# Kernel tuning notes

Measured on AMD Instinct MI355X. Metric: run time of the kernel, lower is better.

Reference implementation:

```python
import jax, jax.numpy as jnp
import numpy as np

B, N, D, H = 256, 64, 128, 64

def _w(key, shape, fan_in):
    return jax.random.normal(key, shape, jnp.float32) * (1.0 / np.sqrt(fan_in))

def setup_inputs() -> dict:
    key = jax.random.key(0)
    ks = jax.random.split(key, 6)
    return {
        "observations": jax.random.normal(ks[0], (B, N, D), jnp.float32),
        "enc_w": _w(ks[1], (D, H), D), "enc_b": jnp.zeros((H,), jnp.float32),
        "gate_w1": _w(ks[2], (2 * H, H), 2 * H), "gate_b1": jnp.zeros((H,), jnp.float32),
        "gate_w2": _w(ks[3], (H, 1), H), "gate_b2": jnp.zeros((1,), jnp.float32),
        "msg_w1": _w(ks[4], (H, H), H), "msg_b1": jnp.zeros((H,), jnp.float32),
        "msg_w2": _w(ks[5], (H, H), H), "msg_b2": jnp.zeros((H,), jnp.float32),
    }

def reference(observations, enc_w, enc_b, gate_w1, gate_b1, gate_w2, gate_b2,
              msg_w1, msg_b1, msg_w2, msg_b2):
    # encoder: (B, N, H)
    enc = jax.nn.relu(observations @ enc_w + enc_b)
    h = enc.shape[-1]
    # gate layer 1 on concat([e_i, e_j]) == e_i @ W_top + e_j @ W_bot; avoids
    # materializing the (B, N, N, 2H) concat tensor.
    w_i, w_j = gate_w1[:h], gate_w1[h:]
    gi = enc @ w_i                       # (B, N, H) contribution of receiver i
    gj = enc @ w_j + gate_b1             # (B, N, H) contribution of sender j
    hid = jax.nn.relu(gi[:, :, None, :] + gj[:, None, :, :])   # (B, N, N, H)
    gates = jax.nn.sigmoid(jnp.squeeze(hid @ gate_w2, -1) + gate_b2[0])  # (B, N, N)
    # message_gen(encoded): identical for every i in the original loop
    msg = jax.nn.relu(enc @ msg_w1 + msg_b1) @ msg_w2 + msg_b2  # (B, N, H)
    # enhanced[b, i] = sum_j gates[b, i, j] * msg[b, j]
    enhanced = jnp.einsum('bij,bjh->bih', gates, msg)           # (B, N, H)
    return enhanced
```

## Files before the change

### kernel.cpp

```cpp
#include <hip/hip_runtime.h>

typedef float  f32x4  __attribute__((ext_vector_type(4)));
typedef short  bf16x8 __attribute__((ext_vector_type(8)));

#define Bb 256

__device__ __forceinline__ uint cvtpk(float lo, float hi) {
    uint r;
    asm("v_cvt_pk_bf16_f32 %0, %1, %2" : "=v"(r) : "v"(lo), "v"(hi));
    return r;
}
__device__ __forceinline__ ushort f2b1(float v) { return (ushort)cvtpk(v, v); }

__device__ __forceinline__ void gl_lds16(const void* g, void* l) {
    __builtin_amdgcn_global_load_lds(
        (const __attribute__((address_space(1))) unsigned int*)g,
        (__attribute__((address_space(3))) unsigned int*)l, 16, 0, 0);
}

union U8 { uint u[4]; bf16x8 v; };

__global__ __launch_bounds__(256) void gcm_prep(
    const float* __restrict__ obs, const float* __restrict__ enc_w,
    const float* __restrict__ gate_w1, const float* __restrict__ msg_w1,
    const float* __restrict__ msg_w2,
    ushort* __restrict__ obs_bf, ushort* __restrict__ wimg)
{
    const int bid = blockIdx.x, t = threadIdx.x;
    if (bid < 1024) {
        const int G  = bid * 256 + t;
        const int e0 = G * 8;
        const int b  = e0 >> 13;
        const int r  = (e0 >> 7) & 63;
        const int d0 = e0 & 127;
        const int ds = d0 ^ ((r & 7) << 3);
        const float* src = obs + (((size_t)b * 64 + r) * 128 + ds);
        float4 f0 = *(const float4*)src;
        float4 f1 = *(const float4*)(src + 4);
        uint4 o;
        o.x = cvtpk(f0.x, f0.y); o.y = cvtpk(f0.z, f0.w);
        o.z = cvtpk(f1.x, f1.y); o.w = cvtpk(f1.z, f1.w);
        *(uint4*)(obs_bf + e0) = o;
    } else {
        const int G  = (bid - 1024) * 256 + t;
        const int e0 = G * 8;
        float v[8];
        if (e0 < 8192) {
            const int n  = e0 >> 7;
            const int k0 = (e0 & 127) ^ ((n & 7) << 3);
            #pragma unroll
            for (int j = 0; j < 8; ++j) v[j] = enc_w[(k0 + j) * 64 + n];
        } else {
            const int e  = e0 - 8192;
            const int n  = e >> 6;
            const int k0 = (e & 63) ^ ((n & 7) << 3);
            const float* base; int col;
            if (n < 64)       { base = gate_w1;           col = n;       }
            else if (n < 128) { base = gate_w1 + 64 * 64; col = n - 64;  }
            else if (n < 192) { base = msg_w1;            col = n - 128; }
            else              { base = msg_w2;            col = n - 192; }
            #pragma unroll
            for (int j = 0; j < 8; ++j) v[j] = base[(k0 + j) * 64 + col];
        }
        uint4 o;
        o.x = cvtpk(v[0], v[1]); o.y = cvtpk(v[2], v[3]);
        o.z = cvtpk(v[4], v[5]); o.w = cvtpk(v[6], v[7]);
        *(uint4*)(wimg + e0) = o;
    }
}

__global__ __launch_bounds__(1024, 1) void gcm_main(
    const ushort* __restrict__ obs_bf, const ushort* __restrict__ wimg,
    const float* __restrict__ enc_b, const float* __restrict__ gate_b1,
    const float* __restrict__ gate_w2, const float* __restrict__ gate_b2,
    const float* __restrict__ msg_b1, const float* __restrict__ msg_b2,
    float* __restrict__ out)
{
    const int bb   = blockIdx.x;
    const int t    = threadIdx.x;
    const int lane = t & 63;
    const int wv   = t >> 6;
    const int lr   = lane & 15;
    const int lg   = lane >> 4;
    const int rt   = wv & 3;
    const int ct   = wv >> 2;

    __shared__ __align__(16) char arena[131072];
    ushort* s_obs    = (ushort*)(arena);
    ushort* s_encwT  = (ushort*)(arena + 16384);
    ushort* s_wT     = (ushort*)(arena + 32768);
    ushort* s_enc    = (ushort*)(arena + 65536);
    ushort* s_msgh   = (ushort*)(arena + 73728);
    float*  s_gi     = (float*) (arena + 81920);
    float*  s_gj     = (float*) (arena + 98304);
    ushort* s_msgT   = (ushort*)(arena + 114688);
    ushort* s_gatesb = (ushort*)(arena + 122880);

    {
        const ushort* ob = obs_bf + (size_t)bb * 8192 + wv * 512 + lane * 8;
        gl_lds16(ob, arena + wv * 1024);
        const ushort* ew = wimg + wv * 512 + lane * 8;
        gl_lds16(ew, arena + 16384 + wv * 1024);
        const ushort* w0 = wimg + 8192 + wv * 512 + lane * 8;
        gl_lds16(w0, arena + 32768 + wv * 1024);
        const ushort* w1 = wimg + 8192 + (wv + 16) * 512 + lane * 8;
        gl_lds16(w1, arena + 32768 + (wv + 16) * 1024);
    }
    __syncthreads();

    {
        f32x4 acc = (f32x4){0.f, 0.f, 0.f, 0.f};
        const int arow = rt * 16 + lr;
        const int n = ct * 16 + lr;
        #pragma unroll
        for (int ks = 0; ks < 4; ++ks) {
            const int k0 = ks * 32 + lg * 8;
            bf16x8 a  = *(const bf16x8*)(s_obs + ((arow * 128 + k0) ^ ((arow & 7) << 3)));
            bf16x8 bf = *(const bf16x8*)(s_encwT + ((n * 128 + k0) ^ ((n & 7) << 3)));
            acc = __builtin_amdgcn_mfma_f32_16x16x32_bf16(a, bf, acc, 0, 0, 0);
        }
        const float be = enc_b[n];
        float v0 = fmaxf(acc[0] + be, 0.f), v1 = fmaxf(acc[1] + be, 0.f);
        float v2 = fmaxf(acc[2] + be, 0.f), v3 = fmaxf(acc[3] + be, 0.f);
        uint pA = cvtpk(v0, v1), pB = cvtpk(v2, v3);
        const int rb = rt * 16 + lg * 4;
        s_enc[((rb + 0) * 64 + n) ^ (((rb + 0) & 7) << 3)] = (ushort)pA;
        s_enc[((rb + 1) * 64 + n) ^ (((rb + 1) & 7) << 3)] = (ushort)(pA >> 16);
        s_enc[((rb + 2) * 64 + n) ^ (((rb + 2) & 7) << 3)] = (ushort)pB;
        s_enc[((rb + 3) * 64 + n) ^ (((rb + 3) & 7) << 3)] = (ushort)(pB >> 16);
    }
    __syncthreads();

    {
        f32x4 acc[3];
        #pragma unroll
        for (int q = 0; q < 3; ++q) acc[q] = (f32x4){0.f, 0.f, 0.f, 0.f};
        const int arow = rt * 16 + lr;
        #pragma unroll
        for (int ks = 0; ks < 2; ++ks) {
            const int k0 = ks * 32 + lg * 8;
            bf16x8 a = *(const bf16x8*)(s_enc + ((arow * 64 + k0) ^ ((arow & 7) << 3)));
            #pragma unroll
            for (int q = 0; q < 3; ++q) {
                const int n = (ct * 3 + q) * 16 + lr;
                bf16x8 bf = *(const bf16x8*)(s_wT + ((n * 64 + k0) ^ ((n & 7) << 3)));
                acc[q] = __builtin_amdgcn_mfma_f32_16x16x32_bf16(a, bf, acc[q], 0, 0, 0);
            }
        }
        const int rb = rt * 16 + lg * 4;
        #pragma unroll
        for (int q = 0; q < 3; ++q) {
            const int nfull = (ct * 3 + q) * 16;
            const int cc = nfull + lr;
            if (nfull < 64) {
                #pragma unroll
                for (int rr = 0; rr < 4; ++rr) {
                    const int row = rb + rr;
                    s_gi[(row * 64 + cc) ^ ((row & 7) << 2)] = acc[q][rr];
                }
            } else if (nfull < 128) {
                const float b1 = gate_b1[cc - 64];
                #pragma unroll
                for (int rr = 0; rr < 4; ++rr) {
                    const int row = rb + rr;
                    s_gj[(row * 64 + (cc - 64)) ^ ((row & 7) << 2)] = acc[q][rr] + b1;
                }
            } else {
                const float bm = msg_b1[cc - 128];
                float v0 = fmaxf(acc[q][0] + bm, 0.f), v1 = fmaxf(acc[q][1] + bm, 0.f);
                float v2 = fmaxf(acc[q][2] + bm, 0.f), v3 = fmaxf(acc[q][3] + bm, 0.f);
                uint pA = cvtpk(v0, v1), pB = cvtpk(v2, v3);
                const int c2 = cc - 128;
                s_msgh[((rb + 0) * 64 + c2) ^ (((rb + 0) & 7) << 3)] = (ushort)pA;
                s_msgh[((rb + 1) * 64 + c2) ^ (((rb + 1) & 7) << 3)] = (ushort)(pA >> 16);
                s_msgh[((rb + 2) * 64 + c2) ^ (((rb + 2) & 7) << 3)] = (ushort)pB;
                s_msgh[((rb + 3) * 64 + c2) ^ (((rb + 3) & 7) << 3)] = (ushort)(pB >> 16);
            }
        }
    }
    __syncthreads();

    {
        f32x4 acc = (f32x4){0.f, 0.f, 0.f, 0.f};
        const int arow = rt * 16 + lr;
        const int nn3 = 192 + ct * 16 + lr;
        #pragma unroll
        for (int ks = 0; ks < 2; ++ks) {
            const int k0 = ks * 32 + lg * 8;
            bf16x8 a  = *(const bf16x8*)(s_msgh + ((arow * 64 + k0) ^ ((arow & 7) << 3)));
            bf16x8 bf = *(const bf16x8*)(s_wT + ((nn3 * 64 + k0) ^ ((nn3 & 7) << 3)));
            acc = __builtin_amdgcn_mfma_f32_16x16x32_bf16(a, bf, acc, 0, 0, 0);
        }
        const int h  = ct * 16 + lr;
        const int jb = rt * 16 + lg * 4;
        const float bm2 = msg_b2[h];
        uint pA = cvtpk(acc[0] + bm2, acc[1] + bm2);
        uint pB = cvtpk(acc[2] + bm2, acc[3] + bm2);
        const int e = (h * 64 + jb) ^ ((h & 7) << 3);
        *(uint*)(s_msgT + e)     = pA;
        *(uint*)(s_msgT + e + 2) = pB;
    }

    {
        const int row0g = wv * 4;
        float ag[4] = {0.f, 0.f, 0.f, 0.f};
        #pragma unroll 4
        for (int h0 = 0; h0 < 64; h0 += 4) {
            float4 gj4 = *(const float4*)&s_gj[(lane * 64 + h0) ^ ((lane & 7) << 2)];
            const float4 w24 = *(const float4*)(gate_w2 + h0);
            #pragma unroll
            for (int r = 0; r < 4; ++r) {
                const int row = row0g + r;
                float4 gi4 = *(const float4*)&s_gi[(row * 64 + h0) ^ ((row & 7) << 2)];
                ag[r] = fmaf(fmaxf(gi4.x + gj4.x, 0.f), w24.x, ag[r]);
                ag[r] = fmaf(fmaxf(gi4.y + gj4.y, 0.f), w24.y, ag[r]);
                ag[r] = fmaf(fmaxf(gi4.z + gj4.z, 0.f), w24.z, ag[r]);
                ag[r] = fmaf(fmaxf(gi4.w + gj4.w, 0.f), w24.w, ag[r]);
            }
        }
        const float b2v = gate_b2[0];
        #pragma unroll
        for (int r = 0; r < 4; ++r) {
            const int row = row0g + r;
            const float g = 1.f / (1.f + __expf(-(ag[r] + b2v)));
            s_gatesb[(row * 64 + lane) ^ ((row & 7) << 3)] = f2b1(g);
        }
    }
    __syncthreads();

    {
        const int rtl = wv >> 2;
        const int ctl = wv & 3;
        f32x4 acc = (f32x4){0.f, 0.f, 0.f, 0.f};
        const int arow = rtl * 16 + lr;
        const int n = ctl * 16 + lr;
        #pragma unroll
        for (int ks = 0; ks < 2; ++ks) {
            const int k0 = ks * 32 + lg * 8;
            bf16x8 a  = *(const bf16x8*)(s_gatesb + ((arow * 64 + k0) ^ ((arow & 7) << 3)));
            bf16x8 bf = *(const bf16x8*)(s_msgT   + ((n * 64 + k0) ^ ((n & 7) << 3)));
            acc = __builtin_amdgcn_mfma_f32_16x16x32_bf16(a, bf, acc, 0, 0, 0);
        }
        const int rb = rtl * 16 + lg * 4;
        #pragma unroll
        for (int rr = 0; rr < 4; ++rr)
            out[((size_t)bb * 64 + rb + rr) * 64 + n] = acc[rr];
    }
}

__global__ __launch_bounds__(1024) void gcm_fb(
    const float* __restrict__ obs, const float* __restrict__ enc_w,
    const float* __restrict__ enc_b, const float* __restrict__ gate_w1,
    const float* __restrict__ gate_b1, const float* __restrict__ gate_w2,
    const float* __restrict__ gate_b2, const float* __restrict__ msg_w1,
    const float* __restrict__ msg_b1, const float* __restrict__ msg_w2,
    const float* __restrict__ msg_b2, float* __restrict__ out)
{
    const int bb   = blockIdx.x;
    const int t    = threadIdx.x;
    const int lane = t & 63;
    const int wv   = t >> 6;
    const int lr   = lane & 15;
    const int lg   = lane >> 4;
    const int rt   = wv & 3;
    const int ct   = wv >> 2;

    __shared__ __align__(16) ushort s_encwT[64 * 128];
    __shared__ __align__(16) ushort s_wT[256 * 64];
    __shared__ __align__(16) ushort s_enc[64 * 64];
    __shared__ __align__(16) ushort s_msgh[64 * 64];
    __shared__ __align__(16) ushort s_gatesb[64 * 64];
    __shared__ __align__(16) ushort s_msgT[64 * 64];
    __shared__ __align__(16) float  s_gi[64 * 64];
    __shared__ __align__(16) float  s_gj[64 * 64];
    __shared__ __align__(16) float  s_w2[64];

    float4 pf[8];
    {
        const float* ob = obs + ((size_t)bb * 64 + rt * 16 + lr) * 128 + lg * 8;
        #pragma unroll
        for (int ks = 0; ks < 4; ++ks) {
            pf[2 * ks]     = *(const float4*)(ob + ks * 32);
            pf[2 * ks + 1] = *(const float4*)(ob + ks * 32 + 4);
        }
    }
    if (t < 64) s_w2[t] = gate_w2[t];
    #pragma unroll
    for (int it = 0; it < 2; ++it) {
        const int g  = t + it * 1024;
        const int k  = g >> 4;
        const int n0 = (g & 15) * 4;
        float4 w4 = *(const float4*)(enc_w + k * 64 + n0);
        uint pA = cvtpk(w4.x, w4.y), pB = cvtpk(w4.z, w4.w);
        s_encwT[((n0 + 0) * 128 + k) ^ (((n0 + 0) & 7) << 3)] = (ushort)pA;
        s_encwT[((n0 + 1) * 128 + k) ^ (((n0 + 1) & 7) << 3)] = (ushort)(pA >> 16);
        s_encwT[((n0 + 2) * 128 + k) ^ (((n0 + 2) & 7) << 3)] = (ushort)pB;
        s_encwT[((n0 + 3) * 128 + k) ^ (((n0 + 3) & 7) << 3)] = (ushort)(pB >> 16);
    }
    bf16x8 afrag[4];
    #pragma unroll
    for (int ks = 0; ks < 4; ++ks) {
        U8 u;
        u.u[0] = cvtpk(pf[2 * ks].x,     pf[2 * ks].y);
        u.u[1] = cvtpk(pf[2 * ks].z,     pf[2 * ks].w);
        u.u[2] = cvtpk(pf[2 * ks + 1].x, pf[2 * ks + 1].y);
        u.u[3] = cvtpk(pf[2 * ks + 1].z, pf[2 * ks + 1].w);
        afrag[ks] = u.v;
    }
    float4 pfw[4];
    {
        const int k  = t >> 4;
        const int n0 = (t & 15) * 4;
        pfw[0] = *(const float4*)(gate_w1 + k * 64 + n0);
        pfw[1] = *(const float4*)(gate_w1 + (64 + k) * 64 + n0);
        pfw[2] = *(const float4*)(msg_w1 + k * 64 + n0);
        pfw[3] = *(const float4*)(msg_w2 + k * 64 + n0);
    }
    __syncthreads();
    {
        f32x4 acc = (f32x4){0.f, 0.f, 0.f, 0.f};
        const int n = ct * 16 + lr;
        #pragma unroll
        for (int ks = 0; ks < 4; ++ks) {
            const int k0 = ks * 32 + lg * 8;
            bf16x8 bf = *(const bf16x8*)(s_encwT + ((n * 128 + k0) ^ ((n & 7) << 3)));
            acc = __builtin_amdgcn_mfma_f32_16x16x32_bf16(afrag[ks], bf, acc, 0, 0, 0);
        }
        #pragma unroll
        for (int it = 0; it < 4; ++it) {
            const int k  = t >> 4;
            const int n0 = it * 64 + (t & 15) * 4;
            uint pA = cvtpk(pfw[it].x, pfw[it].y), pB = cvtpk(pfw[it].z, pfw[it].w);
            s_wT[((n0 + 0) * 64 + k) ^ (((n0 + 0) & 7) << 3)] = (ushort)pA;
            s_wT[((n0 + 1) * 64 + k) ^ (((n0 + 1) & 7) << 3)] = (ushort)(pA >> 16);
            s_wT[((n0 + 2) * 64 + k) ^ (((n0 + 2) & 7) << 3)] = (ushort)pB;
            s_wT[((n0 + 3) * 64 + k) ^ (((n0 + 3) & 7) << 3)] = (ushort)(pB >> 16);
        }
        const float be = enc_b[n];
        float v0 = fmaxf(acc[0] + be, 0.f), v1 = fmaxf(acc[1] + be, 0.f);
        float v2 = fmaxf(acc[2] + be, 0.f), v3 = fmaxf(acc[3] + be, 0.f);
        uint pA = cvtpk(v0, v1), pB = cvtpk(v2, v3);
        const int rb = rt * 16 + lg * 4;
        s_enc[((rb + 0) * 64 + n) ^ (((rb + 0) & 7) << 3)] = (ushort)pA;
        s_enc[((rb + 1) * 64 + n) ^ (((rb + 1) & 7) << 3)] = (ushort)(pA >> 16);
        s_enc[((rb + 2) * 64 + n) ^ (((rb + 2) & 7) << 3)] = (ushort)pB;
        s_enc[((rb + 3) * 64 + n) ^ (((rb + 3) & 7) << 3)] = (ushort)(pB >> 16);
    }
    __syncthreads();
    {
        f32x4 acc[3];
        #pragma unroll
        for (int q = 0; q < 3; ++q) acc[q] = (f32x4){0.f, 0.f, 0.f, 0.f};
        const int arow = rt * 16 + lr;
        #pragma unroll
        for (int ks = 0; ks < 2; ++ks) {
            const int k0 = ks * 32 + lg * 8;
            bf16x8 a = *(const bf16x8*)(s_enc + ((arow * 64 + k0) ^ ((arow & 7) << 3)));
            #pragma unroll
            for (int q = 0; q < 3; ++q) {
                const int n = (ct * 3 + q) * 16 + lr;
                bf16x8 bf = *(const bf16x8*)(s_wT + ((n * 64 + k0) ^ ((n & 7) << 3)));
                acc[q] = __builtin_amdgcn_mfma_f32_16x16x32_bf16(a, bf, acc[q], 0, 0, 0);
            }
        }
        const int rb = rt * 16 + lg * 4;
        #pragma unroll
        for (int q = 0; q < 3; ++q) {
            const int nfull = (ct * 3 + q) * 16;
            const int cc = nfull + lr;
            if (nfull < 64) {
                #pragma unroll
                for (int rr = 0; rr < 4; ++rr) {
                    const int row = rb + rr;
                    s_gi[(row * 64 + cc) ^ ((row & 7) << 2)] = acc[q][rr];
                }
            } else if (nfull < 128) {
                const float b1 = gate_b1[cc - 64];
                #pragma unroll
                for (int rr = 0; rr < 4; ++rr) {
                    const int row = rb + rr;
                    s_gj[(row * 64 + (cc - 64)) ^ ((row & 7) << 2)] = acc[q][rr] + b1;
                }
            } else {
                const float bm = msg_b1[cc - 128];
                float v0 = fmaxf(acc[q][0] + bm, 0.f), v1 = fmaxf(acc[q][1] + bm, 0.f);
                float v2 = fmaxf(acc[q][2] + bm, 0.f), v3 = fmaxf(acc[q][3] + bm, 0.f);
                uint pA = cvtpk(v0, v1), pB = cvtpk(v2, v3);
                const int c2 = cc - 128;
                s_msgh[((rb + 0) * 64 + c2) ^ (((rb + 0) & 7) << 3)] = (ushort)pA;
                s_msgh[((rb + 1) * 64 + c2) ^ (((rb + 1) & 7) << 3)] = (ushort)(pA >> 16);
                s_msgh[((rb + 2) * 64 + c2) ^ (((rb + 2) & 7) << 3)] = (ushort)pB;
                s_msgh[((rb + 3) * 64 + c2) ^ (((rb + 3) & 7) << 3)] = (ushort)(pB >> 16);
            }
        }
    }
    __syncthreads();
    {
        f32x4 acc = (f32x4){0.f, 0.f, 0.f, 0.f};
        const int arow = rt * 16 + lr;
        const int nn3 = 192 + ct * 16 + lr;
        #pragma unroll
        for (int ks = 0; ks < 2; ++ks) {
            const int k0 = ks * 32 + lg * 8;
            bf16x8 a = *(const bf16x8*)(s_msgh + ((arow * 64 + k0) ^ ((arow & 7) << 3)));
            bf16x8 bf = *(const bf16x8*)(s_wT + ((nn3 * 64 + k0) ^ ((nn3 & 7) << 3)));
            acc = __builtin_amdgcn_mfma_f32_16x16x32_bf16(a, bf, acc, 0, 0, 0);
        }
        const int h  = ct * 16 + lr;
        const int jb = rt * 16 + lg * 4;
        const float bm2 = msg_b2[h];
        uint pA = cvtpk(acc[0] + bm2, acc[1] + bm2);
        uint pB = cvtpk(acc[2] + bm2, acc[3] + bm2);
        const int e = (h * 64 + jb) ^ ((h & 7) << 3);
        *(uint*)(s_msgT + e)     = pA;
        *(uint*)(s_msgT + e + 2) = pB;
    }
    {
        const int row0g = wv * 4;
        float ag[4] = {0.f, 0.f, 0.f, 0.f};
        #pragma unroll 4
        for (int h0 = 0; h0 < 64; h0 += 4) {
            float4 gj4 = *(const float4*)&s_gj[(lane * 64 + h0) ^ ((lane & 7) << 2)];
            float4 w24 = *(const float4*)&s_w2[h0];
            #pragma unroll
            for (int r = 0; r < 4; ++r) {
                const int row = row0g + r;
                float4 gi4 = *(const float4*)&s_gi[(row * 64 + h0) ^ ((row & 7) << 2)];
                ag[r] = fmaf(fmaxf(gi4.x + gj4.x, 0.f), w24.x, ag[r]);
                ag[r] = fmaf(fmaxf(gi4.y + gj4.y, 0.f), w24.y, ag[r]);
                ag[r] = fmaf(fmaxf(gi4.z + gj4.z, 0.f), w24.z, ag[r]);
                ag[r] = fmaf(fmaxf(gi4.w + gj4.w, 0.f), w24.w, ag[r]);
            }
        }
        const float b2v = gate_b2[0];
        #pragma unroll
        for (int r = 0; r < 4; ++r) {
            const int row = row0g + r;
            const float g = 1.f / (1.f + __expf(-(ag[r] + b2v)));
            s_gatesb[(row * 64 + lane) ^ ((row & 7) << 3)] = f2b1(g);
        }
    }
    __syncthreads();
    {
        const int rtl = wv >> 2;
        const int ctl = wv & 3;
        f32x4 acc = (f32x4){0.f, 0.f, 0.f, 0.f};
        const int arow = rtl * 16 + lr;
        const int n = ctl * 16 + lr;
        #pragma unroll
        for (int ks = 0; ks < 2; ++ks) {
            const int k0 = ks * 32 + lg * 8;
            bf16x8 a  = *(const bf16x8*)(s_gatesb + ((arow * 64 + k0) ^ ((arow & 7) << 3)));
            bf16x8 bf = *(const bf16x8*)(s_msgT   + ((n * 64 + k0) ^ ((n & 7) << 3)));
            acc = __builtin_amdgcn_mfma_f32_16x16x32_bf16(a, bf, acc, 0, 0, 0);
        }
        const int rb = rtl * 16 + lg * 4;
        #pragma unroll
        for (int rr = 0; rr < 4; ++rr)
            out[((size_t)bb * 64 + rb + rr) * 64 + n] = acc[rr];
    }
}

extern "C" void kernel_launch(void* const* d_in, const int* in_sizes, int n_in,
                              void* d_out, int out_size, void* d_ws, size_t ws_size,
                              hipStream_t stream) {
    const float* obs     = (const float*)d_in[0];
    const float* enc_w   = (const float*)d_in[1];
    const float* enc_b   = (const float*)d_in[2];
    const float* gate_w1 = (const float*)d_in[3];
    const float* gate_b1 = (const float*)d_in[4];
    const float* gate_w2 = (const float*)d_in[5];
    const float* gate_b2 = (const float*)d_in[6];
    const float* msg_w1  = (const float*)d_in[7];
    const float* msg_b1  = (const float*)d_in[8];
    const float* msg_w2  = (const float*)d_in[9];
    const float* msg_b2  = (const float*)d_in[10];
    float* out = (float*)d_out;

    const size_t obs_elems = (size_t)Bb * 64 * 128;
    const size_t w_elems   = 24576;
    const size_t need = (obs_elems + w_elems) * sizeof(ushort);
    if (ws_size >= need) {
        ushort* obs_bf = (ushort*)d_ws;
        ushort* wimg   = obs_bf + obs_elems;
        gcm_prep<<<1036, 256, 0, stream>>>(obs, enc_w, gate_w1, msg_w1, msg_w2,
                                           obs_bf, wimg);
        gcm_main<<<Bb, 1024, 0, stream>>>(obs_bf, wimg, enc_b, gate_b1,
                                          gate_w2, gate_b2, msg_b1, msg_b2, out);
    } else {
        gcm_fb<<<Bb, 1024, 0, stream>>>(obs, enc_w, enc_b, gate_w1, gate_b1,
                                        gate_w2, gate_b2, msg_w1, msg_b1,
                                        msg_w2, msg_b2, out);
    }
}
```

Before: 21.61 us.

## Split each batch across two 512-thread blocks and read operands directly from global

The main kernel now launches two 512-thread blocks per batch element, each producing half of the output rows. Each block recomputes the full encoder and gate/message projections but keeps only its half of the receiver terms. Operands are read straight from global memory into MFMA fragments instead of being staged through LDS with global_load_lds. LDS per block shrinks from 128 KB to 52 KB, which lets several blocks share a CU and should improve occupancy and latency hiding. The cost is duplicated encoder and projection work and more redundant global or cache reads of the weights.

```diff
diff --git a/kernel.cpp b/kernel.cpp
--- a/kernel.cpp
+++ b/kernel.cpp
@@ -11,12 +11,6 @@
     return r;
 }
 __device__ __forceinline__ ushort f2b1(float v) { return (ushort)cvtpk(v, v); }
-
-__device__ __forceinline__ void gl_lds16(const void* g, void* l) {
-    __builtin_amdgcn_global_load_lds(
-        (const __attribute__((address_space(1))) unsigned int*)g,
-        (__attribute__((address_space(3))) unsigned int*)l, 16, 0, 0);
-}
 
 union U8 { uint u[4]; bf16x8 v; };
 
@@ -69,12 +63,204 @@
     }
 }
 
-__global__ __launch_bounds__(1024, 1) void gcm_main(
+__global__ __launch_bounds__(512, 4) void gcm_main(
     const ushort* __restrict__ obs_bf, const ushort* __restrict__ wimg,
     const float* __restrict__ enc_b, const float* __restrict__ gate_b1,
     const float* __restrict__ gate_w2, const float* __restrict__ gate_b2,
     const float* __restrict__ msg_b1, const float* __restrict__ msg_b2,
     float* __restrict__ out)
+{
+    const int bid  = blockIdx.x;
+    const int bb   = bid >> 1;
+    const int half = bid & 1;
+    const int t    = threadIdx.x;
+    const int lane = t & 63;
+    const int wv   = t >> 6;
+    const int lr   = lane & 15;
+    const int lg   = lane >> 4;
+    const int rt   = wv & 3;
+    const int ch   = wv >> 2;
+
+    __shared__ __align__(16) char arena[53248];
+    ushort* s_enc    = (ushort*)(arena);
+    ushort* s_msgh   = (ushort*)(arena + 8192);
+    float*  s_gj     = (float*) (arena + 16384);
+    ushort* s_msgT   = (ushort*)(arena + 32768);
+    float*  s_gi     = (float*) (arena + 40960);
+    ushort* s_gatesb = (ushort*)(arena + 49152);
+
+    {
+        const int arow = rt * 16 + lr;
+        const ushort* ob = obs_bf + (size_t)bb * 8192 + arow * 128;
+        bf16x8 a[4];
+        #pragma unroll
+        for (int ks = 0; ks < 4; ++ks)
+            a[ks] = *(const bf16x8*)(ob + ((ks * 32 + lg * 8) ^ ((arow & 7) << 3)));
+        f32x4 acc[2];
+        acc[0] = (f32x4){0.f, 0.f, 0.f, 0.f};
+        acc[1] = (f32x4){0.f, 0.f, 0.f, 0.f};
+        #pragma unroll
+        for (int jj = 0; jj < 2; ++jj) {
+            const int n = ch * 32 + jj * 16 + lr;
+            const ushort* wp = wimg + n * 128;
+            #pragma unroll
+            for (int ks = 0; ks < 4; ++ks) {
+                bf16x8 bw = *(const bf16x8*)(wp + ((ks * 32 + lg * 8) ^ ((n & 7) << 3)));
+                acc[jj] = __builtin_amdgcn_mfma_f32_16x16x32_bf16(a[ks], bw, acc[jj], 0, 0, 0);
+            }
+        }
+        const int rb = rt * 16 + lg * 4;
+        #pragma unroll
+        for (int jj = 0; jj < 2; ++jj) {
+            const int n = ch * 32 + jj * 16 + lr;
+            const float be = enc_b[n];
+            float v0 = fmaxf(acc[jj][0] + be, 0.f), v1 = fmaxf(acc[jj][1] + be, 0.f);
+            float v2 = fmaxf(acc[jj][2] + be, 0.f), v3 = fmaxf(acc[jj][3] + be, 0.f);
+            uint pA = cvtpk(v0, v1), pB = cvtpk(v2, v3);
+            s_enc[((rb + 0) * 64 + n) ^ (((rb + 0) & 7) << 3)] = (ushort)pA;
+            s_enc[((rb + 1) * 64 + n) ^ (((rb + 1) & 7) << 3)] = (ushort)(pA >> 16);
+            s_enc[((rb + 2) * 64 + n) ^ (((rb + 2) & 7) << 3)] = (ushort)pB;
+            s_enc[((rb + 3) * 64 + n) ^ (((rb + 3) & 7) << 3)] = (ushort)(pB >> 16);
+        }
+    }
+    __syncthreads();
+
+    {
+        const int arow = rt * 16 + lr;
+        bf16x8 a[2];
+        #pragma unroll
+        for (int ks = 0; ks < 2; ++ks)
+            a[ks] = *(const bf16x8*)(s_enc + ((arow * 64 + ks * 32 + lg * 8) ^ ((arow & 7) << 3)));
+        f32x4 acc[6];
+        #pragma unroll
+        for (int q = 0; q < 6; ++q) acc[q] = (f32x4){0.f, 0.f, 0.f, 0.f};
+        #pragma unroll
+        for (int q = 0; q < 6; ++q) {
+            const int n = (ch * 6 + q) * 16 + lr;
+            const ushort* wp = wimg + 8192 + n * 64;
+            #pragma unroll
+            for (int ks = 0; ks < 2; ++ks) {
+                bf16x8 bw = *(const bf16x8*)(wp + ((ks * 32 + lg * 8) ^ ((n & 7) << 3)));
+                acc[q] = __builtin_amdgcn_mfma_f32_16x16x32_bf16(a[ks], bw, acc[q], 0, 0, 0);
+            }
+        }
+        const int rb = rt * 16 + lg * 4;
+        #pragma unroll
+        for (int q = 0; q < 6; ++q) {
+            const int nfull = (ch * 6 + q) * 16;
+            const int cc = nfull + lr;
+            if (nfull < 64) {
+                if ((rt >> 1) == half) {
+                    const int lb = rb - half * 32;
+                    #pragma unroll
+                    for (int rr = 0; rr < 4; ++rr) {
+                        const int row = lb + rr;
+                        s_gi[(row * 64 + cc) ^ ((row & 7) << 2)] = acc[q][rr];
+                    }
+                }
+            } else if (nfull < 128) {
+                const float b1 = gate_b1[cc - 64];
+                #pragma unroll
+                for (int rr = 0; rr < 4; ++rr) {
+                    const int row = rb + rr;
+                    s_gj[(row * 64 + (cc - 64)) ^ ((row & 7) << 2)] = acc[q][rr] + b1;
+                }
+            } else {
+                const float bm = msg_b1[cc - 128];
+                float v0 = fmaxf(acc[q][0] + bm, 0.f), v1 = fmaxf(acc[q][1] + bm, 0.f);
+                float v2 = fmaxf(acc[q][2] + bm, 0.f), v3 = fmaxf(acc[q][3] + bm, 0.f);
+                uint pA = cvtpk(v0, v1), pB = cvtpk(v2, v3);
+                const int c2 = cc - 128;
+                s_msgh[((rb + 0) * 64 + c2) ^ (((rb + 0) & 7) << 3)] = (ushort)pA;
+                s_msgh[((rb + 1) * 64 + c2) ^ (((rb + 1) & 7) << 3)] = (ushort)(pA >> 16);
+                s_msgh[((rb + 2) * 64 + c2) ^ (((rb + 2) & 7) << 3)] = (ushort)pB;
+                s_msgh[((rb + 3) * 64 + c2) ^ (((rb + 3) & 7) << 3)] = (ushort)(pB >> 16);
+            }
+        }
+    }
+    __syncthreads();
+
+    {
+        const int arow = rt * 16 + lr;
+        bf16x8 a[2];
+        #pragma unroll
+        for (int ks = 0; ks < 2; ++ks)
+            a[ks] = *(const bf16x8*)(s_msgh + ((arow * 64 + ks * 32 + lg * 8) ^ ((arow & 7) << 3)));
+        #pragma unroll
+        for (int jj = 0; jj < 2; ++jj) {
+            const int n = 192 + ch * 32 + jj * 16 + lr;
+            const ushort* wp = wimg + 8192 + n * 64;
+            f32x4 acc = (f32x4){0.f, 0.f, 0.f, 0.f};
+            #pragma unroll
+            for (int ks = 0; ks < 2; ++ks) {
+                bf16x8 bw = *(const bf16x8*)(wp + ((ks * 32 + lg * 8) ^ ((n & 7) << 3)));
+                acc = __builtin_amdgcn_mfma_f32_16x16x32_bf16(a[ks], bw, acc, 0, 0, 0);
+            }
+            const int h  = ch * 32 + jj * 16 + lr;
+            const int jb = rt * 16 + lg * 4;
+            const float bm2 = msg_b2[h];
+            uint pA = cvtpk(acc[0] + bm2, acc[1] + bm2);
+            uint pB = cvtpk(acc[2] + bm2, acc[3] + bm2);
+            const int e = (h * 64 + jb) ^ ((h & 7) << 3);
+            *(uint*)(s_msgT + e)     = pA;
+            *(uint*)(s_msgT + e + 2) = pB;
+        }
+    }
+
+    {
+        const int lrow0 = wv * 4;
+        float ag[4] = {0.f, 0.f, 0.f, 0.f};
+        #pragma unroll 4
+        for (int h0 = 0; h0 < 64; h0 += 4) {
+            float4 gj4 = *(const float4*)&s_gj[(lane * 64 + h0) ^ ((lane & 7) << 2)];
+            const float4 w24 = *(const float4*)(gate_w2 + h0);
+            #pragma unroll
+            for (int r = 0; r < 4; ++r) {
+                const int row = lrow0 + r;
+                float4 gi4 = *(const float4*)&s_gi[(row * 64 + h0) ^ ((row & 7) << 2)];
+                ag[r] = fmaf(fmaxf(gi4.x + gj4.x, 0.f), w24.x, ag[r]);
+                ag[r] = fmaf(fmaxf(gi4.y + gj4.y, 0.f), w24.y, ag[r]);
+                ag[r] = fmaf(fmaxf(gi4.z + gj4.z, 0.f), w24.z, ag[r]);
+                ag[r] = fmaf(fmaxf(gi4.w + gj4.w, 0.f), w24.w, ag[r]);
+            }
+        }
+        const float b2v = gate_b2[0];
+        #pragma unroll
+        for (int r = 0; r < 4; ++r) {
+            const int row = lrow0 + r;
+            const float g = 1.f / (1.f + __expf(-(ag[r] + b2v)));
+            s_gatesb[(row * 64 + lane) ^ ((row & 7) << 3)] = f2b1(g);
+        }
+    }
+    __syncthreads();
+
+    {
+        const int rtl = wv >> 2;
+        const int ctl = wv & 3;
+        f32x4 acc = (f32x4){0.f, 0.f, 0.f, 0.f};
+        const int arow = rtl * 16 + lr;
+        const int n = ctl * 16 + lr;
+        #pragma unroll
+        for (int ks = 0; ks < 2; ++ks) {
+            const int k0 = ks * 32 + lg * 8;
+            bf16x8 a  = *(const bf16x8*)(s_gatesb + ((arow * 64 + k0) ^ ((arow & 7) << 3)));
+            bf16x8 bf = *(const bf16x8*)(s_msgT   + ((n * 64 + k0) ^ ((n & 7) << 3)));
+            acc = __builtin_amdgcn_mfma_f32_16x16x32_bf16(a, bf, acc, 0, 0, 0);
+        }
+        const int rb = half * 32 + rtl * 16 + lg * 4;
+        #pragma unroll
+        for (int rr = 0; rr < 4; ++rr)
+            out[((size_t)bb * 64 + rb + rr) * 64 + n] = acc[rr];
+    }
+}
+
+__global__ __launch_bounds__(1024) void gcm_fb(
+    const float* __restrict__ obs, const float* __restrict__ enc_w,
+    const float* __restrict__ enc_b, const float* __restrict__ gate_w1,
+    const float* __restrict__ gate_b1, const float* __restrict__ gate_w2,
+    const float* __restrict__ gate_b2, const float* __restrict__ msg_w1,
+    const float* __restrict__ msg_b1, const float* __restrict__ msg_w2,
+    const float* __restrict__ msg_b2, float* __restrict__ out)
 {
     const int bb   = blockIdx.x;
     const int t    = threadIdx.x;
@@ -85,39 +271,76 @@
     const int rt   = wv & 3;
     const int ct   = wv >> 2;
 
-    __shared__ __align__(16) char arena[131072];
-    ushort* s_obs    = (ushort*)(arena);
-    ushort* s_encwT  = (ushort*)(arena + 16384);
-    ushort* s_wT     = (ushort*)(arena + 32768);
-    ushort* s_enc    = (ushort*)(arena + 65536);
-    ushort* s_msgh   = (ushort*)(arena + 73728);
-    float*  s_gi     = (float*) (arena + 81920);
-    float*  s_gj     = (float*) (arena + 98304);
-    ushort* s_msgT   = (ushort*)(arena + 114688);
-    ushort* s_gatesb = (ushort*)(arena + 122880);
-
-    {
-        const ushort* ob = obs_bf + (size_t)bb * 8192 + wv * 512 + lane * 8;
-        gl_lds16(ob, arena + wv * 1024);
-        const ushort* ew = wimg + wv * 512 + lane * 8;
-        gl_lds16(ew, arena + 16384 + wv * 1024);
-        const ushort* w0 = wimg + 8192 + wv * 512 + lane * 8;
-        gl_lds16(w0, arena + 32768 + wv * 1024);
-        const ushort* w1 = wimg + 8192 + (wv + 16) * 512 + lane * 8;
-        gl_lds16(w1, arena + 32768 + (wv + 16) * 1024);
-    }
-    __syncthreads();
-
+    __shared__ __align__(16) ushort s_encwT[64 * 128];
+    __shared__ __align__(16) ushort s_wT[256 * 64];
+    __shared__ __align__(16) ushort s_enc[64 * 64];
+    __shared__ __align__(16) ushort s_msgh[64 * 64];
+    __shared__ __align__(16) ushort s_gatesb[64 * 64];
+    __shared__ __align__(16) ushort s_msgT[64 * 64];
+    __shared__ __align__(16) float  s_gi[64 * 64];
+    __shared__ __align__(16) float  s_gj[64 * 64];
+    __shared__ __align__(16) float  s_w2[64];
+
+    float4 pf[8];
+    {
+        const float* ob = obs + ((size_t)bb * 64 + rt * 16 + lr) * 128 + lg * 8;
+        #pragma unroll
+        for (int ks = 0; ks < 4; ++ks) {
+            pf[2 * ks]     = *(const float4*)(ob + ks * 32);
+            pf[2 * ks + 1] = *(const float4*)(ob + ks * 32 + 4);
+        }
+    }
+    if (t < 64) s_w2[t] = gate_w2[t];
+    #pragma unroll
+    for (int it = 0; it < 2; ++it) {
+        const int g  = t + it * 1024;
+        const int k  = g >> 4;
+        const int n0 = (g & 15) * 4;
+        float4 w4 = *(const float4*)(enc_w + k * 64 + n0);
+        uint pA = cvtpk(w4.x, w4.y), pB = cvtpk(w4.z, w4.w);
+        s_encwT[((n0 + 0) * 128 + k) ^ (((n0 + 0) & 7) << 3)] = (ushort)pA;
+        s_encwT[((n0 + 1) * 128 + k) ^ (((n0 + 1) & 7) << 3)] = (ushort)(pA >> 16);
+        s_encwT[((n0 + 2) * 128 + k) ^ (((n0 + 2) & 7) << 3)] = (ushort)pB;
+        s_encwT[((n0 + 3) * 128 + k) ^ (((n0 + 3) & 7) << 3)] = (ushort)(pB >> 16);
+    }
+    bf16x8 afrag[4];
+    #pragma unroll
+    for (int ks = 0; ks < 4; ++ks) {
+        U8 u;
+        u.u[0] = cvtpk(pf[2 * ks].x,     pf[2 * ks].y);
+        u.u[1] = cvtpk(pf[2 * ks].z,     pf[2 * ks].w);
+        u.u[2] = cvtpk(pf[2 * ks + 1].x, pf[2 * ks + 1].y);
+        u.u[3] = cvtpk(pf[2 * ks + 1].z, pf[2 * ks + 1].w);
+        afrag[ks] = u.v;
+    }
+    float4 pfw[4];
+    {
+        const int k  = t >> 4;
+        const int n0 = (t & 15) * 4;
+        pfw[0] = *(const float4*)(gate_w1 + k * 64 + n0);
+        pfw[1] = *(const float4*)(gate_w1 + (64 + k) * 64 + n0);
+        pfw[2] = *(const float4*)(msg_w1 + k * 64 + n0);
+        pfw[3] = *(const float4*)(msg_w2 + k * 64 + n0);
+    }
+    __syncthreads();
     {
         f32x4 acc = (f32x4){0.f, 0.f, 0.f, 0.f};
-        const int arow = rt * 16 + lr;
         const int n = ct * 16 + lr;
         #pragma unroll
         for (int ks = 0; ks < 4; ++ks) {
             const int k0 = ks * 32 + lg * 8;
-            bf16x8 a  = *(const bf16x8*)(s_obs + ((arow * 128 + k0) ^ ((arow & 7) << 3)));
             bf16x8 bf = *(const bf16x8*)(s_encwT + ((n * 128 + k0) ^ ((n & 7) << 3)));
-            acc = __builtin_amdgcn_mfma_f32_16x16x32_bf16(a, bf, acc, 0, 0, 0);
+            acc = __builtin_amdgcn_mfma_f32_16x16x32_bf16(afrag[ks], bf, acc, 0, 0, 0);
+        }
+        #pragma unroll
+        for (int it = 0; it < 4; ++it) {
+            const int k  = t >> 4;
+            const int n0 = it * 64 + (t & 15) * 4;
+            uint pA = cvtpk(pfw[it].x, pfw[it].y), pB = cvtpk(pfw[it].z, pfw[it].w);
+            s_wT[((n0 + 0) * 64 + k) ^ (((n0 + 0) & 7) << 3)] = (ushort)pA;
+            s_wT[((n0 + 1) * 64 + k) ^ (((n0 + 1) & 7) << 3)] = (ushort)(pA >> 16);
+            s_wT[((n0 + 2) * 64 + k) ^ (((n0 + 2) & 7) << 3)] = (ushort)pB;
+            s_wT[((n0 + 3) * 64 + k) ^ (((n0 + 3) & 7) << 3)] = (ushort)(pB >> 16);
         }
         const float be = enc_b[n];
         float v0 = fmaxf(acc[0] + be, 0.f), v1 = fmaxf(acc[1] + be, 0.f);
@@ -130,7 +353,6 @@
         s_enc[((rb + 3) * 64 + n) ^ (((rb + 3) & 7) << 3)] = (ushort)(pB >> 16);
     }
     __syncthreads();
-
     {
         f32x4 acc[3];
         #pragma unroll
@@ -179,222 +401,6 @@
         }
     }
     __syncthreads();
-
-    {
-        f32x4 acc = (f32x4){0.f, 0.f, 0.f, 0.f};
-        const int arow = rt * 16 + lr;
-        const int nn3 = 192 + ct * 16 + lr;
-        #pragma unroll
-        for (int ks = 0; ks < 2; ++ks) {
-            const int k0 = ks * 32 + lg * 8;
-            bf16x8 a  = *(const bf16x8*)(s_msgh + ((arow * 64 + k0) ^ ((arow & 7) << 3)));
-            bf16x8 bf = *(const bf16x8*)(s_wT + ((nn3 * 64 + k0) ^ ((nn3 & 7) << 3)));
-            acc = __builtin_amdgcn_mfma_f32_16x16x32_bf16(a, bf, acc, 0, 0, 0);
-        }
-        const int h  = ct * 16 + lr;
-        const int jb = rt * 16 + lg * 4;
-        const float bm2 = msg_b2[h];
-        uint pA = cvtpk(acc[0] + bm2, acc[1] + bm2);
-        uint pB = cvtpk(acc[2] + bm2, acc[3] + bm2);
-        const int e = (h * 64 + jb) ^ ((h & 7) << 3);
-        *(uint*)(s_msgT + e)     = pA;
-        *(uint*)(s_msgT + e + 2) = pB;
-    }
-
-    {
-        const int row0g = wv * 4;
-        float ag[4] = {0.f, 0.f, 0.f, 0.f};
-        #pragma unroll 4
-        for (int h0 = 0; h0 < 64; h0 += 4) {
-            float4 gj4 = *(const float4*)&s_gj[(lane * 64 + h0) ^ ((lane & 7) << 2)];
-            const float4 w24 = *(const float4*)(gate_w2 + h0);
-            #pragma unroll
-            for (int r = 0; r < 4; ++r) {
-                const int row = row0g + r;
-                float4 gi4 = *(const float4*)&s_gi[(row * 64 + h0) ^ ((row & 7) << 2)];
-                ag[r] = fmaf(fmaxf(gi4.x + gj4.x, 0.f), w24.x, ag[r]);
-                ag[r] = fmaf(fmaxf(gi4.y + gj4.y, 0.f), w24.y, ag[r]);
-                ag[r] = fmaf(fmaxf(gi4.z + gj4.z, 0.f), w24.z, ag[r]);
-                ag[r] = fmaf(fmaxf(gi4.w + gj4.w, 0.f), w24.w, ag[r]);
-            }
-        }
-        const float b2v = gate_b2[0];
-        #pragma unroll
-        for (int r = 0; r < 4; ++r) {
-            const int row = row0g + r;
-            const float g = 1.f / (1.f + __expf(-(ag[r] + b2v)));
-            s_gatesb[(row * 64 + lane) ^ ((row & 7) << 3)] = f2b1(g);
-        }
-    }
-    __syncthreads();
-
-    {
-        const int rtl = wv >> 2;
-        const int ctl = wv & 3;
-        f32x4 acc = (f32x4){0.f, 0.f, 0.f, 0.f};
-        const int arow = rtl * 16 + lr;
-        const int n = ctl * 16 + lr;
-        #pragma unroll
-        for (int ks = 0; ks < 2; ++ks) {
-            const int k0 = ks * 32 + lg * 8;
-            bf16x8 a  = *(const bf16x8*)(s_gatesb + ((arow * 64 + k0) ^ ((arow & 7) << 3)));
-            bf16x8 bf = *(const bf16x8*)(s_msgT   + ((n * 64 + k0) ^ ((n & 7) << 3)));
-            acc = __builtin_amdgcn_mfma_f32_16x16x32_bf16(a, bf, acc, 0, 0, 0);
-        }
-        const int rb = rtl * 16 + lg * 4;
-        #pragma unroll
-        for (int rr = 0; rr < 4; ++rr)
-            out[((size_t)bb * 64 + rb + rr) * 64 + n] = acc[rr];
-    }
-}
-
-__global__ __launch_bounds__(1024) void gcm_fb(
-    const float* __restrict__ obs, const float* __restrict__ enc_w,
-    const float* __restrict__ enc_b, const float* __restrict__ gate_w1,
-    const float* __restrict__ gate_b1, const float* __restrict__ gate_w2,
-    const float* __restrict__ gate_b2, const float* __restrict__ msg_w1,
-    const float* __restrict__ msg_b1, const float* __restrict__ msg_w2,
-    const float* __restrict__ msg_b2, float* __restrict__ out)
-{
-    const int bb   = blockIdx.x;
-    const int t    = threadIdx.x;
-    const int lane = t & 63;
-    const int wv   = t >> 6;
-    const int lr   = lane & 15;
-    const int lg   = lane >> 4;
-    const int rt   = wv & 3;
-    const int ct   = wv >> 2;
-
-    __shared__ __align__(16) ushort s_encwT[64 * 128];
-    __shared__ __align__(16) ushort s_wT[256 * 64];
-    __shared__ __align__(16) ushort s_enc[64 * 64];
-    __shared__ __align__(16) ushort s_msgh[64 * 64];
-    __shared__ __align__(16) ushort s_gatesb[64 * 64];
-    __shared__ __align__(16) ushort s_msgT[64 * 64];
-    __shared__ __align__(16) float  s_gi[64 * 64];
-    __shared__ __align__(16) float  s_gj[64 * 64];
-    __shared__ __align__(16) float  s_w2[64];
-
-    float4 pf[8];
-    {
-        const float* ob = obs + ((size_t)bb * 64 + rt * 16 + lr) * 128 + lg * 8;
-        #pragma unroll
-        for (int ks = 0; ks < 4; ++ks) {
-            pf[2 * ks]     = *(const float4*)(ob + ks * 32);
-            pf[2 * ks + 1] = *(const float4*)(ob + ks * 32 + 4);
-        }
-    }
-    if (t < 64) s_w2[t] = gate_w2[t];
-    #pragma unroll
-    for (int it = 0; it < 2; ++it) {
-        const int g  = t + it * 1024;
-        const int k  = g >> 4;
-        const int n0 = (g & 15) * 4;
-        float4 w4 = *(const float4*)(enc_w + k * 64 + n0);
-        uint pA = cvtpk(w4.x, w4.y), pB = cvtpk(w4.z, w4.w);
-        s_encwT[((n0 + 0) * 128 + k) ^ (((n0 + 0) & 7) << 3)] = (ushort)pA;
-        s_encwT[((n0 + 1) * 128 + k) ^ (((n0 + 1) & 7) << 3)] = (ushort)(pA >> 16);
-        s_encwT[((n0 + 2) * 128 + k) ^ (((n0 + 2) & 7) << 3)] = (ushort)pB;
-        s_encwT[((n0 + 3) * 128 + k) ^ (((n0 + 3) & 7) << 3)] = (ushort)(pB >> 16);
-    }
-    bf16x8 afrag[4];
-    #pragma unroll
-    for (int ks = 0; ks < 4; ++ks) {
-        U8 u;
-        u.u[0] = cvtpk(pf[2 * ks].x,     pf[2 * ks].y);
-        u.u[1] = cvtpk(pf[2 * ks].z,     pf[2 * ks].w);
-        u.u[2] = cvtpk(pf[2 * ks + 1].x, pf[2 * ks + 1].y);
-        u.u[3] = cvtpk(pf[2 * ks + 1].z, pf[2 * ks + 1].w);
-        afrag[ks] = u.v;
-    }
-    float4 pfw[4];
-    {
-        const int k  = t >> 4;
-        const int n0 = (t & 15) * 4;
-        pfw[0] = *(const float4*)(gate_w1 + k * 64 + n0);
-        pfw[1] = *(const float4*)(gate_w1 + (64 + k) * 64 + n0);
-        pfw[2] = *(const float4*)(msg_w1 + k * 64 + n0);
-        pfw[3] = *(const float4*)(msg_w2 + k * 64 + n0);
-    }
-    __syncthreads();
-    {
-        f32x4 acc = (f32x4){0.f, 0.f, 0.f, 0.f};
-        const int n = ct * 16 + lr;
-        #pragma unroll
-        for (int ks = 0; ks < 4; ++ks) {
-            const int k0 = ks * 32 + lg * 8;
-            bf16x8 bf = *(const bf16x8*)(s_encwT + ((n * 128 + k0) ^ ((n & 7) << 3)));
-            acc = __builtin_amdgcn_mfma_f32_16x16x32_bf16(afrag[ks], bf, acc, 0, 0, 0);
-        }
-        #pragma unroll
-        for (int it = 0; it < 4; ++it) {
-            const int k  = t >> 4;
-            const int n0 = it * 64 + (t & 15) * 4;
-            uint pA = cvtpk(pfw[it].x, pfw[it].y), pB = cvtpk(pfw[it].z, pfw[it].w);
-            s_wT[((n0 + 0) * 64 + k) ^ (((n0 + 0) & 7) << 3)] = (ushort)pA;
-            s_wT[((n0 + 1) * 64 + k) ^ (((n0 + 1) & 7) << 3)] = (ushort)(pA >> 16);
-            s_wT[((n0 + 2) * 64 + k) ^ (((n0 + 2) & 7) << 3)] = (ushort)pB;
-            s_wT[((n0 + 3) * 64 + k) ^ (((n0 + 3) & 7) << 3)] = (ushort)(pB >> 16);
-        }
-        const float be = enc_b[n];
-        float v0 = fmaxf(acc[0] + be, 0.f), v1 = fmaxf(acc[1] + be, 0.f);
-        float v2 = fmaxf(acc[2] + be, 0.f), v3 = fmaxf(acc[3] + be, 0.f);
-        uint pA = cvtpk(v0, v1), pB = cvtpk(v2, v3);
-        const int rb = rt * 16 + lg * 4;
-        s_enc[((rb + 0) * 64 + n) ^ (((rb + 0) & 7) << 3)] = (ushort)pA;
-        s_enc[((rb + 1) * 64 + n) ^ (((rb + 1) & 7) << 3)] = (ushort)(pA >> 16);
-        s_enc[((rb + 2) * 64 + n) ^ (((rb + 2) & 7) << 3)] = (ushort)pB;
-        s_enc[((rb + 3) * 64 + n) ^ (((rb + 3) & 7) << 3)] = (ushort)(pB >> 16);
-    }
-    __syncthreads();
-    {
-        f32x4 acc[3];
-        #pragma unroll
-        for (int q = 0; q < 3; ++q) acc[q] = (f32x4){0.f, 0.f, 0.f, 0.f};
-        const int arow = rt * 16 + lr;
-        #pragma unroll
-        for (int ks = 0; ks < 2; ++ks) {
-            const int k0 = ks * 32 + lg * 8;
-            bf16x8 a = *(const bf16x8*)(s_enc + ((arow * 64 + k0) ^ ((arow & 7) << 3)));
-            #pragma unroll
-            for (int q = 0; q < 3; ++q) {
-                const int n = (ct * 3 + q) * 16 + lr;
-                bf16x8 bf = *(const bf16x8*)(s_wT + ((n * 64 + k0) ^ ((n & 7) << 3)));
-                acc[q] = __builtin_amdgcn_mfma_f32_16x16x32_bf16(a, bf, acc[q], 0, 0, 0);
-            }
-        }
-        const int rb = rt * 16 + lg * 4;
-        #pragma unroll
-        for (int q = 0; q < 3; ++q) {
-            const int nfull = (ct * 3 + q) * 16;
-            const int cc = nfull + lr;
-            if (nfull < 64) {
-                #pragma unroll
-                for (int rr = 0; rr < 4; ++rr) {
-                    const int row = rb + rr;
-                    s_gi[(row * 64 + cc) ^ ((row & 7) << 2)] = acc[q][rr];
-                }
-            } else if (nfull < 128) {
-                const float b1 = gate_b1[cc - 64];
-                #pragma unroll
-                for (int rr = 0; rr < 4; ++rr) {
-                    const int row = rb + rr;
-                    s_gj[(row * 64 + (cc - 64)) ^ ((row & 7) << 2)] = acc[q][rr] + b1;
-                }
-            } else {
-                const float bm = msg_b1[cc - 128];
-                float v0 = fmaxf(acc[q][0] + bm, 0.f), v1 = fmaxf(acc[q][1] + bm, 0.f);
-                float v2 = fmaxf(acc[q][2] + bm, 0.f), v3 = fmaxf(acc[q][3] + bm, 0.f);
-                uint pA = cvtpk(v0, v1), pB = cvtpk(v2, v3);
-                const int c2 = cc - 128;
-                s_msgh[((rb + 0) * 64 + c2) ^ (((rb + 0) & 7) << 3)] = (ushort)pA;
-                s_msgh[((rb + 1) * 64 + c2) ^ (((rb + 1) & 7) << 3)] = (ushort)(pA >> 16);
-                s_msgh[((rb + 2) * 64 + c2) ^ (((rb + 2) & 7) << 3)] = (ushort)pB;
-                s_msgh[((rb + 3) * 64 + c2) ^ (((rb + 3) & 7) << 3)] = (ushort)(pB >> 16);
-            }
-        }
-    }
-    __syncthreads();
     {
         f32x4 acc = (f32x4){0.f, 0.f, 0.f, 0.f};
         const int arow = rt * 16 + lr;
@@ -485,8 +491,8 @@
         ushort* wimg   = obs_bf + obs_elems;
         gcm_prep<<<1036, 256, 0, stream>>>(obs, enc_w, gate_w1, msg_w1, msg_w2,
                                            obs_bf, wimg);
-        gcm_main<<<Bb, 1024, 0, stream>>>(obs_bf, wimg, enc_b, gate_b1,
-                                          gate_w2, gate_b2, msg_b1, msg_b2, out);
+        gcm_main<<<2 * Bb, 512, 0, stream>>>(obs_bf, wimg, enc_b, gate_b1,
+                                             gate_w2, gate_b2, msg_b1, msg_b2, out);
     } else {
         gcm_fb<<<Bb, 1024, 0, stream>>>(obs, enc_w, enc_b, gate_w1, gate_b1,
                                         gate_w2, gate_b2, msg_w1, msg_b1,
```

Result: slower. 24.56 us (+13.7%).
